# Performance work log

Measured on AMD Instinct MI355X. Metric: run time of the kernel, lower is better.

The kernel has to match this reference:

```python
import jax, jax.numpy as jnp
import numpy as np

BSZ, E, D, R = 8, 40000, 128, 512
NUM_STEPS, K, DEG = 2, 3, 64
T = E * DEG  # uniform out-degree KB
M = K * DEG  # max gathered triples per example per step


def setup_inputs() -> dict:
    key = jax.random.key(0)
    ks = jax.random.split(key, 10)
    s = 1.0 / np.sqrt(D)
    start_idx = jax.random.randint(ks[0], (BSZ,), 0, E)
    start = jnp.zeros((BSZ, E), jnp.float32).at[jnp.arange(BSZ), start_idx].set(1.0)
    query = jax.random.randint(ks[1], (BSZ,), 0, R)
    sub = jnp.repeat(jnp.arange(E), DEG)
    obj = jax.random.randint(ks[2], (T,), 0, E)
    rel = jax.random.randint(ks[3], (T,), 0, R)
    kb_triple = jnp.stack([sub, obj, rel], axis=1)  # [T,3] = (sub, obj, rel)
    kb_range = jnp.stack([jnp.arange(E) * DEG, (jnp.arange(E) + 1) * DEG], axis=1)
    rel_emb = jax.random.normal(ks[4], (R, D), jnp.float32) * s
    step_W = jax.random.normal(ks[5], (NUM_STEPS, D, D), jnp.float32) * np.sqrt(2.0 / D)
    step_b = jnp.zeros((NUM_STEPS, D), jnp.float32)
    gru_W_ih = jax.random.normal(ks[6], (3 * D, D), jnp.float32) * s
    gru_W_hh = jax.random.normal(ks[7], (3 * D, D), jnp.float32) * s
    gru_b_ih = jnp.zeros((3 * D,), jnp.float32)
    gru_b_hh = jnp.zeros((3 * D,), jnp.float32)
    cls_w = jax.random.normal(ks[8], (D,), jnp.float32) * np.sqrt(2.0 / D)
    cls_b = jnp.zeros((1,), jnp.float32)
    return dict(start=start, rel_emb=rel_emb, step_W=step_W, step_b=step_b,
                gru_W_ih=gru_W_ih, gru_W_hh=gru_W_hh, gru_b_ih=gru_b_ih, gru_b_hh=gru_b_hh,
                cls_w=cls_w, cls_b=cls_b, query=query, kb_triple=kb_triple, kb_range=kb_range)


def _gru_cell(x, h, W_ih, W_hh, b_ih, b_hh):
    # torch GRU cell, gate order (r, z, n). x, h: [..., D]
    gi = x @ W_ih.T + b_ih
    gh = h @ W_hh.T + b_hh
    i_r, i_z, i_n = jnp.split(gi, 3, axis=-1)
    h_r, h_z, h_n = jnp.split(gh, 3, axis=-1)
    r = jax.nn.sigmoid(i_r + h_r)
    z = jax.nn.sigmoid(i_z + h_z)
    n = jnp.tanh(i_n + r * h_n)
    return (1.0 - z) * n + z * h


def _forward(start, rel_emb, step_W, step_b, gru_W_ih, gru_W_hh, gru_b_ih, gru_b_hh,
             cls_w, cls_b, query, kb_triple, kb_range):
    bsz, nE = start.shape
    d = rel_emb.shape[1]
    q_emb = rel_emb[query]                       # [bsz, D]
    last_e = start
    hist = jnp.zeros((bsz, nE, d), start.dtype)  # [bsz, E, D]
    for t in range(NUM_STEPS):
        cq = jnp.tanh(q_emb @ step_W[t] + step_b[t])           # [bsz, D]
        _, top_idx = jax.lax.top_k(last_e, K)                  # [bsz, K]
        n_valid = 1 if t == 0 else K                           # topk=1 at step 0
        ent_mask = jnp.arange(K) < n_valid                     # [K]
        lo = kb_range[top_idx, 0]                              # [bsz, K]
        hi = kb_range[top_idx, 1]
        tri_idx = lo[..., None] + jnp.arange(DEG)              # [bsz, K, DEG]
        valid = (tri_idx < hi[..., None]) & ent_mask[None, :, None]
        tri_idx = jnp.where(valid, tri_idx, 0).reshape(bsz, M)
        valid = valid.reshape(bsz, M).astype(start.dtype)
        trip = kb_triple[tri_idx]                              # [bsz, M, 3]
        sub, obj, rel = trip[..., 0], trip[..., 1], trip[..., 2]
        sub_feat = jnp.take_along_axis(hist, sub[..., None], axis=1)   # [bsz, M, D]
        rel_feat = rel_emb[rel]                                        # [bsz, M, D]
        trans = _gru_cell(rel_feat, sub_feat, gru_W_ih, gru_W_hh, gru_b_ih, gru_b_hh)
        trans_prob = jax.nn.sigmoid(jnp.einsum('bmd,d->bm', trans * cq[:, None, :], cls_w) + cls_b[0])
        sub_p = jnp.take_along_axis(last_e, sub, axis=1)       # [bsz, M]
        obj_p = sub_p * trans_prob * valid                     # masked transition prob
        last_e = jax.vmap(lambda o, p: jnp.zeros((nE,), p.dtype).at[o].add(p))(obj, obj_p)
        obj_feat = trans * obj_p[..., None]
        hist = jax.vmap(lambda o, f: jnp.zeros((nE, d), f.dtype).at[o].add(f))(obj, obj_feat)
        zdiv = jax.lax.stop_gradient(jnp.where(last_e > 1.0, last_e, 1.0))
        last_e = last_e / zdiv
    return last_e


def reference(start, rel_emb, step_W, step_b, gru_W_ih, gru_W_hh, gru_b_ih, gru_b_hh,
              cls_w, cls_b, query, kb_triple, kb_range):
    return _forward(start, rel_emb, step_W, step_b, gru_W_ih, gru_W_hh, gru_b_ih, gru_b_hh,
                    cls_w, cls_b, query, kb_triple, kb_range)
```

## Files before the change

kernel.cpp:

```cpp
#include <hip/hip_runtime.h>
#include <math.h>

#define BSZ 8
#define E_ENT 40000
#define D_DIM 128
#define K_TOP 3
#define DEG 64
#define M_TRI (K_TOP * DEG)
#define D3 (3 * D_DIM)
#define NCH 40
#define CHUNK 1000

#define ZERO_BLOCKS 313
#define TR_BLOCKS 192
#define CQ_BLOCKS (2 * BSZ)
#define SA_BLOCKS (BSZ * NCH)
#define PREP_BLOCKS (ZERO_BLOCKS + TR_BLOCKS + CQ_BLOCKS + SA_BLOCKS)

typedef unsigned long long ull;

__device__ __forceinline__ float sigmoidf_(float x) { return 1.0f / (1.0f + expf(-x)); }

__device__ __forceinline__ ull make_key(float v, int idx) {
    return ((ull)__float_as_uint(v) << 32) |
           (ull)(0xFFFFFFFFu - (unsigned int)idx);
}
__device__ __forceinline__ int key_idx(ull k) {
    return (int)(0xFFFFFFFFu - (unsigned int)(k & 0xFFFFFFFFull));
}
__device__ __forceinline__ float key_val(ull k) {
    return __uint_as_float((unsigned int)(k >> 32));
}

__global__ void prep_kernel(const float* __restrict__ start,
                            const float* __restrict__ rel_emb,
                            const float* __restrict__ step_W,
                            const float* __restrict__ step_b,
                            const int* __restrict__ query,
                            const float* __restrict__ W_ih,
                            const float* __restrict__ W_hh,
                            float* __restrict__ WT_ih,
                            float* __restrict__ WT_hh,
                            float* __restrict__ cq,
                            ull* __restrict__ keysA,
                            float* __restrict__ out) {
    int blk = blockIdx.x, tid = threadIdx.x;
    __shared__ float xs[D_DIM];
    __shared__ ull red[256];
    if (blk < ZERO_BLOCKS) {
        int i = blk * 256 + tid;
        if (i < (BSZ * E_ENT) / 4) ((float4*)out)[i] = float4{0.f, 0.f, 0.f, 0.f};
    } else if (blk < ZERO_BLOCKS + TR_BLOCKS) {
        int i = (blk - ZERO_BLOCKS) * 256 + tid;
        int row = i / D_DIM, col = i % D_DIM;
        WT_ih[col * D3 + row] = W_ih[row * D_DIM + col];
        WT_hh[col * D3 + row] = W_hh[row * D_DIM + col];
    } else if (blk < ZERO_BLOCKS + TR_BLOCKS + CQ_BLOCKS) {
        int g = blk - (ZERO_BLOCKS + TR_BLOCKS);
        int t = g / BSZ, b = g % BSZ;
        if (tid < D_DIM) xs[tid] = rel_emb[query[b] * D_DIM + tid];
        __syncthreads();
        if (tid < D_DIM) {
            float acc = step_b[t * D_DIM + tid];
            const float* W = step_W + t * D_DIM * D_DIM;
            for (int k = 0; k < D_DIM; k++) acc += xs[k] * W[k * D_DIM + tid];
            cq[(t * BSZ + b) * D_DIM + tid] = tanhf(acc);
        }
    } else {
        int g = blk - (ZERO_BLOCKS + TR_BLOCKS + CQ_BLOCKS);
        int b = g / NCH, c = g % NCH;
        const float* row = start + (size_t)b * E_ENT;
        int base = c * CHUNK;
        ull best = 0ull;
        for (int i = tid; i < CHUNK; i += 256) {
            int idx = base + i;
            ull k = make_key(row[idx], idx);
            if (k > best) best = k;
        }
        red[tid] = best;
        __syncthreads();
        for (int s = 128; s > 0; s >>= 1) {
            if (tid < s && red[tid + s] > red[tid]) red[tid] = red[tid + s];
            __syncthreads();
        }
        if (tid == 0) keysA[b * NCH + c] = red[0];
    }
}

__global__ __launch_bounds__(128) void step0_kernel(
        const ull* __restrict__ keysA,
        const float* __restrict__ cq,
        const float* __restrict__ rel_emb,
        const int* __restrict__ kb_triple,
        const int* __restrict__ kb_range,
        const float* __restrict__ WT_ih,
        const float* __restrict__ b_ih,
        const float* __restrict__ b_hh,
        const float* __restrict__ cls_w,
        const float* __restrict__ cls_b,
        float* __restrict__ feat_out,
        int* __restrict__ obj_out,
        float* __restrict__ p_out) {
    int blk = blockIdx.x;
    int b = blk / DEG, j = blk % DEG;
    int d = threadIdx.x;

    __shared__ ull kred[64];
    __shared__ float xs[D_DIM];
    __shared__ float red[D_DIM];

    if (d < 64) kred[d] = (d < NCH) ? keysA[b * NCH + d] : 0ull;
    __syncthreads();
    for (int s = 32; s > 0; s >>= 1) {
        if (d < s && kred[d + s] > kred[d]) kred[d] = kred[d + s];
        __syncthreads();
    }
    int ent = key_idx(kred[0]);
    float sub_p = key_val(kred[0]);
    int lo = kb_range[2 * ent], hi = kb_range[2 * ent + 1];
    int tri = lo + j;
    bool vj = tri < hi;
    int tuse = vj ? tri : 0;
    int obj = kb_triple[3 * tuse + 1];
    int rel = kb_triple[3 * tuse + 2];

    xs[d] = rel_emb[rel * D_DIM + d];
    __syncthreads();

    float ir = b_ih[d], iz = b_ih[D_DIM + d], inn = b_ih[2 * D_DIM + d];
    for (int kk = 0; kk < D_DIM; kk++) {
        const float* wi = WT_ih + kk * D3;
        float xk = xs[kk];
        ir += xk * wi[d]; iz += xk * wi[D_DIM + d]; inn += xk * wi[2 * D_DIM + d];
    }
    float r = sigmoidf_(ir + b_hh[d]);
    float z = sigmoidf_(iz + b_hh[D_DIM + d]);
    float n = tanhf(inn + r * b_hh[2 * D_DIM + d]);
    float trans = (1.f - z) * n;

    red[d] = trans * cq[b * D_DIM + d] * cls_w[d];
    __syncthreads();
    for (int s = 64; s > 0; s >>= 1) {
        if (d < s) red[d] += red[d + s];
        __syncthreads();
    }
    float prob = sigmoidf_(red[0] + cls_b[0]);
    float obj_p = vj ? sub_p * prob : 0.f;

    feat_out[((size_t)b * DEG + j) * D_DIM + d] = trans * obj_p;
    if (d == 0) { obj_out[b * DEG + j] = obj; p_out[b * DEG + j] = obj_p; }
}

__global__ __launch_bounds__(128) void step1_kernel(
        const int* __restrict__ objs,
        const float* __restrict__ p0,
        const float* __restrict__ feat_in,
        const float* __restrict__ cq,
        const float* __restrict__ rel_emb,
        const int* __restrict__ kb_triple,
        const int* __restrict__ kb_range,
        const float* __restrict__ WT_ih,
        const float* __restrict__ WT_hh,
        const float* __restrict__ b_ih,
        const float* __restrict__ b_hh,
        const float* __restrict__ cls_w,
        const float* __restrict__ cls_b,
        int* __restrict__ obj_out,
        float* __restrict__ p_out) {
    int blk = blockIdx.x;
    int b = blk / (K_TOP * DEG);
    int rem = blk % (K_TOP * DEG);
    int k = rem / DEG, j = rem % DEG;
    int d = threadIdx.x;

    __shared__ int so[DEG];
    __shared__ float sp[DEG];
    __shared__ ull kred[64];
    __shared__ int pick_i[K_TOP];
    __shared__ float pick_v[K_TOP];
    __shared__ float hds[D_DIM];
    __shared__ float xs[D_DIM];
    __shared__ float red[D_DIM];

    if (d < DEG) { so[d] = objs[b * DEG + d]; sp[d] = p0[b * DEG + d]; }
    __syncthreads();

    ull mykey = 0ull; int myobj = -1;
    if (d < DEG) {
        myobj = so[d];
        float v = 0.f;
        for (int i = 0; i < DEG; i++) if (so[i] == myobj) v += sp[i];
        v = v / fmaxf(v, 1.f);
        mykey = make_key(v, myobj);
    }
    for (int p = 0; p < K_TOP; p++) {
        ull k2 = mykey;
        for (int q = 0; q < p; q++) if (myobj == pick_i[q]) k2 = 0ull;
        if (d < 64) kred[d] = k2;
        __syncthreads();
        for (int s = 32; s > 0; s >>= 1) {
            if (d < s && kred[d + s] > kred[d]) kred[d] = kred[d + s];
            __syncthreads();
        }
        if (d == 0) {
            int idx = key_idx(kred[0]);
            float val = key_val(kred[0]);
            if (idx < 0 || idx >= E_ENT) { idx = p; val = 0.f; }
            pick_i[p] = idx; pick_v[p] = val;
        }
        __syncthreads();
    }
    int ent = pick_i[k];
    float sub_p = pick_v[k];

    float hd = 0.f;
    for (int m = 0; m < DEG; m++)
        if (so[m] == ent) hd += feat_in[((size_t)b * DEG + m) * D_DIM + d];
    hds[d] = hd;

    int lo = kb_range[2 * ent], hi = kb_range[2 * ent + 1];
    int tri = lo + j;
    bool vj = tri < hi;
    int tuse = vj ? tri : 0;
    int obj = kb_triple[3 * tuse + 1];
    int rel = kb_triple[3 * tuse + 2];
    xs[d] = rel_emb[rel * D_DIM + d];
    __syncthreads();

    float ir = b_ih[d], iz = b_ih[D_DIM + d], inn = b_ih[2 * D_DIM + d];
    float hr = b_hh[d], hz = b_hh[D_DIM + d], hn = b_hh[2 * D_DIM + d];
    for (int kk = 0; kk < D_DIM; kk++) {
        const float* wi = WT_ih + kk * D3;
        const float* wh = WT_hh + kk * D3;
        float xk = xs[kk], hk = hds[kk];
        ir += xk * wi[d]; iz += xk * wi[D_DIM + d]; inn += xk * wi[2 * D_DIM + d];
        hr += hk * wh[d]; hz += hk * wh[D_DIM + d]; hn += hk * wh[2 * D_DIM + d];
    }
    float r = sigmoidf_(ir + hr);
    float z = sigmoidf_(iz + hz);
    float n = tanhf(inn + r * hn);
    float trans = (1.f - z) * n + z * hd;

    red[d] = trans * cq[b * D_DIM + d] * cls_w[d];
    __syncthreads();
    for (int s = 64; s > 0; s >>= 1) {
        if (d < s) red[d] += red[d + s];
        __syncthreads();
    }
    float prob = sigmoidf_(red[0] + cls_b[0]);
    if (d == 0) {
        int idx = b * M_TRI + k * DEG + j;
        obj_out[idx] = obj;
        p_out[idx] = vj ? sub_p * prob : 0.f;
    }
}

__global__ void finalize_kernel(const int* __restrict__ obj1,
                                const float* __restrict__ p1,
                                float* __restrict__ out) {
    int b = blockIdx.x, m = threadIdx.x;
    __shared__ int so[M_TRI];
    __shared__ float sp[M_TRI];
    so[m] = obj1[b * M_TRI + m];
    sp[m] = p1[b * M_TRI + m];
    __syncthreads();
    int o = so[m];
    float v = 0.f;
    for (int i = 0; i < M_TRI; i++) if (so[i] == o) v += sp[i];
    out[(size_t)b * E_ENT + o] = v / fmaxf(v, 1.f);
}

extern "C" void kernel_launch(void* const* d_in, const int* in_sizes, int n_in,
                              void* d_out, int out_size, void* d_ws, size_t ws_size,
                              hipStream_t stream) {
    const float* start    = (const float*)d_in[0];
    const float* rel_emb  = (const float*)d_in[1];
    const float* step_W   = (const float*)d_in[2];
    const float* step_b   = (const float*)d_in[3];
    const float* W_ih     = (const float*)d_in[4];
    const float* W_hh     = (const float*)d_in[5];
    const float* b_ih     = (const float*)d_in[6];
    const float* b_hh     = (const float*)d_in[7];
    const float* cls_w    = (const float*)d_in[8];
    const float* cls_b    = (const float*)d_in[9];
    const int*   query    = (const int*)d_in[10];
    const int*   kb_triple = (const int*)d_in[11];
    const int*   kb_range  = (const int*)d_in[12];
    float* out = (float*)d_out;

    char* ws = (char*)d_ws;
    float* WT_ih = (float*)ws;  ws += (size_t)D3 * D_DIM * sizeof(float);
    float* WT_hh = (float*)ws;  ws += (size_t)D3 * D_DIM * sizeof(float);
    float* cq    = (float*)ws;  ws += (size_t)2 * BSZ * D_DIM * sizeof(float);
    float* feat  = (float*)ws;  ws += (size_t)BSZ * DEG * D_DIM * sizeof(float);
    int*   objs  = (int*)ws;    ws += (size_t)BSZ * DEG * sizeof(int);
    float* p0    = (float*)ws;  ws += (size_t)BSZ * DEG * sizeof(float);
    ull*   keysA = (ull*)ws;    ws += (size_t)BSZ * NCH * sizeof(ull);
    int*   obj1  = (int*)ws;    ws += (size_t)BSZ * M_TRI * sizeof(int);
    float* p1    = (float*)ws;  ws += (size_t)BSZ * M_TRI * sizeof(float);

    prep_kernel<<<PREP_BLOCKS, 256, 0, stream>>>(
        start, rel_emb, step_W, step_b, query, W_ih, W_hh,
        WT_ih, WT_hh, cq, keysA, out);

    step0_kernel<<<BSZ * DEG, 128, 0, stream>>>(
        keysA, cq, rel_emb, kb_triple, kb_range,
        WT_ih, b_ih, b_hh, cls_w, cls_b,
        feat, objs, p0);

    step1_kernel<<<BSZ * K_TOP * DEG, 128, 0, stream>>>(
        objs, p0, feat, cq + BSZ * D_DIM, rel_emb, kb_triple, kb_range,
        WT_ih, WT_hh, b_ih, b_hh, cls_w, cls_b,
        obj1, p1);

    finalize_kernel<<<BSZ, M_TRI, 0, stream>>>(obj1, p1, out);
}
```

Baseline: 60.02 us.

## Fuse finalize into step1 via last-block counter and batch triples per block

Removes the separate finalize launch: each step1 block bumps a per-example atomic counter, and the last block for that example does the scatter and normalize into the output. Step1 now handles all three top-k entities in one 384-thread block, so the top-k selection is computed once per (b,j) rather than three times. Step0 packs two triples per 256-thread block. The dot-product reductions use wave shuffles in place of shared-memory trees. The cost is a threadfence and atomic on the tail, plus a counter reset added to the prep kernel.

```diff
diff --git a/kernel.cpp b/kernel.cpp
--- a/kernel.cpp
+++ b/kernel.cpp
@@ -11,11 +11,10 @@
 #define NCH 40
 #define CHUNK 1000
 
-#define ZERO_BLOCKS 313
-#define TR_BLOCKS 192
-#define CQ_BLOCKS (2 * BSZ)
-#define SA_BLOCKS (BSZ * NCH)
-#define PREP_BLOCKS (ZERO_BLOCKS + TR_BLOCKS + CQ_BLOCKS + SA_BLOCKS)
+#define PZ 313
+#define PT_END (PZ + 192)
+#define PC_END (PT_END + 16)
+#define PS_END (PC_END + 320)
 
 typedef unsigned long long ull;
 
@@ -32,32 +31,35 @@
     return __uint_as_float((unsigned int)(k >> 32));
 }
 
-__global__ void prep_kernel(const float* __restrict__ start,
-                            const float* __restrict__ rel_emb,
-                            const float* __restrict__ step_W,
-                            const float* __restrict__ step_b,
-                            const int* __restrict__ query,
-                            const float* __restrict__ W_ih,
-                            const float* __restrict__ W_hh,
-                            float* __restrict__ WT_ih,
-                            float* __restrict__ WT_hh,
-                            float* __restrict__ cq,
-                            ull* __restrict__ keysA,
-                            float* __restrict__ out) {
+__global__ __launch_bounds__(256) void prep_kernel(
+        const float* __restrict__ start,
+        const float* __restrict__ rel_emb,
+        const float* __restrict__ step_W,
+        const float* __restrict__ step_b,
+        const int* __restrict__ query,
+        const float* __restrict__ W_ih,
+        const float* __restrict__ W_hh,
+        float* __restrict__ WT_ih,
+        float* __restrict__ WT_hh,
+        float* __restrict__ cq,
+        ull* __restrict__ keysA,
+        int* __restrict__ cnt,
+        float* __restrict__ out) {
     int blk = blockIdx.x, tid = threadIdx.x;
     __shared__ float xs[D_DIM];
     __shared__ ull red[256];
-    if (blk < ZERO_BLOCKS) {
+    if (blk < PZ) {
+        if (blk == 0 && tid < BSZ) cnt[tid] = 0;
         int i = blk * 256 + tid;
         if (i < (BSZ * E_ENT) / 4) ((float4*)out)[i] = float4{0.f, 0.f, 0.f, 0.f};
-    } else if (blk < ZERO_BLOCKS + TR_BLOCKS) {
-        int i = (blk - ZERO_BLOCKS) * 256 + tid;
-        int row = i / D_DIM, col = i % D_DIM;
-        WT_ih[col * D3 + row] = W_ih[row * D_DIM + col];
-        WT_hh[col * D3 + row] = W_hh[row * D_DIM + col];
-    } else if (blk < ZERO_BLOCKS + TR_BLOCKS + CQ_BLOCKS) {
-        int g = blk - (ZERO_BLOCKS + TR_BLOCKS);
-        int t = g / BSZ, b = g % BSZ;
+    } else if (blk < PT_END) {
+        int i = (blk - PZ) * 256 + tid;
+        int row = i >> 7, col = i & 127;
+        WT_ih[col * D3 + row] = W_ih[i];
+        WT_hh[col * D3 + row] = W_hh[i];
+    } else if (blk < PC_END) {
+        int g = blk - PT_END;
+        int t = g >> 3, b = g & 7;
         if (tid < D_DIM) xs[tid] = rel_emb[query[b] * D_DIM + tid];
         __syncthreads();
         if (tid < D_DIM) {
@@ -67,14 +69,13 @@
             cq[(t * BSZ + b) * D_DIM + tid] = tanhf(acc);
         }
     } else {
-        int g = blk - (ZERO_BLOCKS + TR_BLOCKS + CQ_BLOCKS);
+        int g = blk - PC_END;
         int b = g / NCH, c = g % NCH;
         const float* row = start + (size_t)b * E_ENT;
         int base = c * CHUNK;
         ull best = 0ull;
         for (int i = tid; i < CHUNK; i += 256) {
-            int idx = base + i;
-            ull k = make_key(row[idx], idx);
+            ull k = make_key(row[base + i], base + i);
             if (k > best) best = k;
         }
         red[tid] = best;
@@ -87,7 +88,7 @@
     }
 }
 
-__global__ __launch_bounds__(128) void step0_kernel(
+__global__ __launch_bounds__(256) void step0_kernel(
         const ull* __restrict__ keysA,
         const float* __restrict__ cq,
         const float* __restrict__ rel_emb,
@@ -98,21 +99,22 @@
         const float* __restrict__ b_hh,
         const float* __restrict__ cls_w,
         const float* __restrict__ cls_b,
-        float* __restrict__ feat_out,
-        int* __restrict__ obj_out,
-        float* __restrict__ p_out) {
-    int blk = blockIdx.x;
-    int b = blk / DEG, j = blk % DEG;
-    int d = threadIdx.x;
+        float* __restrict__ feat,
+        int* __restrict__ objs,
+        float* __restrict__ p0) {
+    int blk = blockIdx.x, tid = threadIdx.x;
+    int b = blk >> 5, jj = blk & 31;
+    int e = tid >> 7, d = tid & 127, j = jj * 2 + e;
 
     __shared__ ull kred[64];
-    __shared__ float xs[D_DIM];
-    __shared__ float red[D_DIM];
-
-    if (d < 64) kred[d] = (d < NCH) ? keysA[b * NCH + d] : 0ull;
+    __shared__ float s_x[2][D_DIM];
+    __shared__ float s_part[2][2];
+    __shared__ float s_prob[2];
+
+    if (tid < 64) kred[tid] = (tid < NCH) ? keysA[b * NCH + tid] : 0ull;
     __syncthreads();
     for (int s = 32; s > 0; s >>= 1) {
-        if (d < s && kred[d + s] > kred[d]) kred[d] = kred[d + s];
+        if (tid < s && kred[tid + s] > kred[tid]) kred[tid] = kred[tid + s];
         __syncthreads();
     }
     int ent = key_idx(kred[0]);
@@ -120,17 +122,16 @@
     int lo = kb_range[2 * ent], hi = kb_range[2 * ent + 1];
     int tri = lo + j;
     bool vj = tri < hi;
-    int tuse = vj ? tri : 0;
-    int obj = kb_triple[3 * tuse + 1];
-    int rel = kb_triple[3 * tuse + 2];
-
-    xs[d] = rel_emb[rel * D_DIM + d];
+    int tu = vj ? tri : 0;
+    int obj = kb_triple[3 * tu + 1];
+    int rel = kb_triple[3 * tu + 2];
+    s_x[e][d] = rel_emb[rel * D_DIM + d];
     __syncthreads();
 
     float ir = b_ih[d], iz = b_ih[D_DIM + d], inn = b_ih[2 * D_DIM + d];
     for (int kk = 0; kk < D_DIM; kk++) {
         const float* wi = WT_ih + kk * D3;
-        float xk = xs[kk];
+        float xk = s_x[e][kk];
         ir += xk * wi[d]; iz += xk * wi[D_DIM + d]; inn += xk * wi[2 * D_DIM + d];
     }
     float r = sigmoidf_(ir + b_hh[d]);
@@ -138,23 +139,22 @@
     float n = tanhf(inn + r * b_hh[2 * D_DIM + d]);
     float trans = (1.f - z) * n;
 
-    red[d] = trans * cq[b * D_DIM + d] * cls_w[d];
-    __syncthreads();
-    for (int s = 64; s > 0; s >>= 1) {
-        if (d < s) red[d] += red[d + s];
-        __syncthreads();
-    }
-    float prob = sigmoidf_(red[0] + cls_b[0]);
-    float obj_p = vj ? sub_p * prob : 0.f;
-
-    feat_out[((size_t)b * DEG + j) * D_DIM + d] = trans * obj_p;
-    if (d == 0) { obj_out[b * DEG + j] = obj; p_out[b * DEG + j] = obj_p; }
-}
-
-__global__ __launch_bounds__(128) void step1_kernel(
+    float v = trans * cq[b * D_DIM + d] * cls_w[d];
+    for (int off = 32; off > 0; off >>= 1) v += __shfl_xor(v, off, 64);
+    if ((tid & 63) == 0) s_part[e][(tid >> 6) & 1] = v;
+    __syncthreads();
+    if (tid < 2) s_prob[tid] = sigmoidf_(s_part[tid][0] + s_part[tid][1] + cls_b[0]);
+    __syncthreads();
+    float obj_p = vj ? sub_p * s_prob[e] : 0.f;
+
+    feat[((size_t)b * DEG + j) * D_DIM + d] = trans * obj_p;
+    if (d == 0) { objs[b * DEG + j] = obj; p0[b * DEG + j] = obj_p; }
+}
+
+__global__ __launch_bounds__(384) void step1_kernel(
         const int* __restrict__ objs,
         const float* __restrict__ p0,
-        const float* __restrict__ feat_in,
+        const float* __restrict__ feat,
         const float* __restrict__ cq,
         const float* __restrict__ rel_emb,
         const int* __restrict__ kb_triple,
@@ -165,66 +165,70 @@
         const float* __restrict__ b_hh,
         const float* __restrict__ cls_w,
         const float* __restrict__ cls_b,
-        int* __restrict__ obj_out,
-        float* __restrict__ p_out) {
-    int blk = blockIdx.x;
-    int b = blk / (K_TOP * DEG);
-    int rem = blk % (K_TOP * DEG);
-    int k = rem / DEG, j = rem % DEG;
-    int d = threadIdx.x;
-
-    __shared__ int so[DEG];
-    __shared__ float sp[DEG];
+        int* __restrict__ obj1,
+        float* __restrict__ p1,
+        int* __restrict__ cnt,
+        float* __restrict__ out) {
+    int blk = blockIdx.x, tid = threadIdx.x;
+    int b = blk >> 6, j = blk & 63;
+    int k = tid >> 7, d = tid & 127;
+
+    __shared__ int s_so[DEG];
+    __shared__ float s_sp[DEG];
     __shared__ ull kred[64];
-    __shared__ int pick_i[K_TOP];
-    __shared__ float pick_v[K_TOP];
-    __shared__ float hds[D_DIM];
-    __shared__ float xs[D_DIM];
-    __shared__ float red[D_DIM];
-
-    if (d < DEG) { so[d] = objs[b * DEG + d]; sp[d] = p0[b * DEG + d]; }
+    __shared__ int s_pi[K_TOP];
+    __shared__ float s_pv[K_TOP];
+    __shared__ float s_x[K_TOP][D_DIM];
+    __shared__ float s_h[K_TOP][D_DIM];
+    __shared__ float s_part[K_TOP][2];
+    __shared__ float s_prob[K_TOP];
+    __shared__ int s_last;
+    __shared__ int s_fo[M_TRI];
+    __shared__ float s_fp[M_TRI];
+
+    if (tid < DEG) { s_so[tid] = objs[b * DEG + tid]; s_sp[tid] = p0[b * DEG + tid]; }
     __syncthreads();
 
     ull mykey = 0ull; int myobj = -1;
-    if (d < DEG) {
-        myobj = so[d];
+    if (tid < DEG) {
+        myobj = s_so[tid];
         float v = 0.f;
-        for (int i = 0; i < DEG; i++) if (so[i] == myobj) v += sp[i];
+        for (int i = 0; i < DEG; i++) if (s_so[i] == myobj) v += s_sp[i];
         v = v / fmaxf(v, 1.f);
         mykey = make_key(v, myobj);
     }
     for (int p = 0; p < K_TOP; p++) {
         ull k2 = mykey;
-        for (int q = 0; q < p; q++) if (myobj == pick_i[q]) k2 = 0ull;
-        if (d < 64) kred[d] = k2;
+        for (int q = 0; q < p; q++) if (myobj == s_pi[q]) k2 = 0ull;
+        if (tid < 64) kred[tid] = k2;
         __syncthreads();
         for (int s = 32; s > 0; s >>= 1) {
-            if (d < s && kred[d + s] > kred[d]) kred[d] = kred[d + s];
+            if (tid < s && kred[tid + s] > kred[tid]) kred[tid] = kred[tid + s];
             __syncthreads();
         }
-        if (d == 0) {
+        if (tid == 0) {
             int idx = key_idx(kred[0]);
             float val = key_val(kred[0]);
             if (idx < 0 || idx >= E_ENT) { idx = p; val = 0.f; }
-            pick_i[p] = idx; pick_v[p] = val;
-        }
-        __syncthreads();
-    }
-    int ent = pick_i[k];
-    float sub_p = pick_v[k];
+            s_pi[p] = idx; s_pv[p] = val;
+        }
+        __syncthreads();
+    }
+    int ent = s_pi[k];
+    float sub_p = s_pv[k];
 
     float hd = 0.f;
     for (int m = 0; m < DEG; m++)
-        if (so[m] == ent) hd += feat_in[((size_t)b * DEG + m) * D_DIM + d];
-    hds[d] = hd;
+        if (s_so[m] == ent) hd += feat[((size_t)b * DEG + m) * D_DIM + d];
+    s_h[k][d] = hd;
 
     int lo = kb_range[2 * ent], hi = kb_range[2 * ent + 1];
     int tri = lo + j;
     bool vj = tri < hi;
-    int tuse = vj ? tri : 0;
-    int obj = kb_triple[3 * tuse + 1];
-    int rel = kb_triple[3 * tuse + 2];
-    xs[d] = rel_emb[rel * D_DIM + d];
+    int tu = vj ? tri : 0;
+    int obj = kb_triple[3 * tu + 1];
+    int rel = kb_triple[3 * tu + 2];
+    s_x[k][d] = rel_emb[rel * D_DIM + d];
     __syncthreads();
 
     float ir = b_ih[d], iz = b_ih[D_DIM + d], inn = b_ih[2 * D_DIM + d];
@@ -232,7 +236,7 @@
     for (int kk = 0; kk < D_DIM; kk++) {
         const float* wi = WT_ih + kk * D3;
         const float* wh = WT_hh + kk * D3;
-        float xk = xs[kk], hk = hds[kk];
+        float xk = s_x[k][kk], hk = s_h[k][kk];
         ir += xk * wi[d]; iz += xk * wi[D_DIM + d]; inn += xk * wi[2 * D_DIM + d];
         hr += hk * wh[d]; hz += hk * wh[D_DIM + d]; hn += hk * wh[2 * D_DIM + d];
     }
@@ -241,33 +245,35 @@
     float n = tanhf(inn + r * hn);
     float trans = (1.f - z) * n + z * hd;
 
-    red[d] = trans * cq[b * D_DIM + d] * cls_w[d];
-    __syncthreads();
-    for (int s = 64; s > 0; s >>= 1) {
-        if (d < s) red[d] += red[d + s];
-        __syncthreads();
-    }
-    float prob = sigmoidf_(red[0] + cls_b[0]);
+    float v = trans * cq[(BSZ + b) * D_DIM + d] * cls_w[d];
+    for (int off = 32; off > 0; off >>= 1) v += __shfl_xor(v, off, 64);
+    if ((tid & 63) == 0) s_part[k][(tid >> 6) & 1] = v;
+    __syncthreads();
+    if (tid < K_TOP) s_prob[tid] = sigmoidf_(s_part[tid][0] + s_part[tid][1] + cls_b[0]);
+    __syncthreads();
     if (d == 0) {
         int idx = b * M_TRI + k * DEG + j;
-        obj_out[idx] = obj;
-        p_out[idx] = vj ? sub_p * prob : 0.f;
-    }
-}
-
-__global__ void finalize_kernel(const int* __restrict__ obj1,
-                                const float* __restrict__ p1,
-                                float* __restrict__ out) {
-    int b = blockIdx.x, m = threadIdx.x;
-    __shared__ int so[M_TRI];
-    __shared__ float sp[M_TRI];
-    so[m] = obj1[b * M_TRI + m];
-    sp[m] = p1[b * M_TRI + m];
-    __syncthreads();
-    int o = so[m];
-    float v = 0.f;
-    for (int i = 0; i < M_TRI; i++) if (so[i] == o) v += sp[i];
-    out[(size_t)b * E_ENT + o] = v / fmaxf(v, 1.f);
+        obj1[idx] = obj;
+        p1[idx] = vj ? sub_p * s_prob[k] : 0.f;
+    }
+
+    __syncthreads();
+    if (tid == 0) {
+        __threadfence();
+        s_last = (atomicAdd(&cnt[b], 1) == DEG - 1);
+    }
+    __syncthreads();
+    if (!s_last) return;
+    __threadfence();
+
+    if (tid < M_TRI) { s_fo[tid] = obj1[b * M_TRI + tid]; s_fp[tid] = p1[b * M_TRI + tid]; }
+    __syncthreads();
+    if (tid < M_TRI) {
+        int o = s_fo[tid];
+        float vv = 0.f;
+        for (int i = 0; i < M_TRI; i++) if (s_fo[i] == o) vv += s_fp[i];
+        out[(size_t)b * E_ENT + o] = vv / fmaxf(vv, 1.f);
+    }
 }
 
 extern "C" void kernel_launch(void* const* d_in, const int* in_sizes, int n_in,
@@ -298,20 +304,19 @@
     ull*   keysA = (ull*)ws;    ws += (size_t)BSZ * NCH * sizeof(ull);
     int*   obj1  = (int*)ws;    ws += (size_t)BSZ * M_TRI * sizeof(int);
     float* p1    = (float*)ws;  ws += (size_t)BSZ * M_TRI * sizeof(float);
-
-    prep_kernel<<<PREP_BLOCKS, 256, 0, stream>>>(
+    int*   cnt   = (int*)ws;    ws += (size_t)BSZ * sizeof(int);
+
+    prep_kernel<<<PS_END, 256, 0, stream>>>(
         start, rel_emb, step_W, step_b, query, W_ih, W_hh,
-        WT_ih, WT_hh, cq, keysA, out);
-
-    step0_kernel<<<BSZ * DEG, 128, 0, stream>>>(
+        WT_ih, WT_hh, cq, keysA, cnt, out);
+
+    step0_kernel<<<BSZ * 32, 256, 0, stream>>>(
         keysA, cq, rel_emb, kb_triple, kb_range,
         WT_ih, b_ih, b_hh, cls_w, cls_b,
         feat, objs, p0);
 
-    step1_kernel<<<BSZ * K_TOP * DEG, 128, 0, stream>>>(
-        objs, p0, feat, cq + BSZ * D_DIM, rel_emb, kb_triple, kb_range,
+    step1_kernel<<<BSZ * DEG, 384, 0, stream>>>(
+        objs, p0, feat, cq, rel_emb, kb_triple, kb_range,
         WT_ih, WT_hh, b_ih, b_hh, cls_w, cls_b,
-        obj1, p1);
-
-    finalize_kernel<<<BSZ, M_TRI, 0, stream>>>(obj1, p1, out);
-}
+        obj1, p1, cnt, out);
+}
```

Result: slower. 72.41 us (+20.7%).
